# Kernel tuning notes

Hardware: AMD Instinct MI355X
Metric: run time of the kernel (lower is better)

The kernel has to match this reference:

```python
import jax, jax.numpy as jnp
import numpy as np
from jax import lax

B, T, V, E, H, L = 512, 128, 128, 512, 512, 2  # batch, seq, vocab, embd, hidden, layers


def setup_inputs() -> dict:
    key = jax.random.key(0)
    ks = jax.random.split(key, 6)
    s = 1.0 / np.sqrt(H)
    return {
        "input": jax.random.randint(ks[0], (B, T), 0, V),
        "encoder_curr_state": jnp.zeros((L, B, H), dtype=jnp.float32),
        "emb": jax.random.normal(ks[1], (V, E), dtype=jnp.float32) * 0.02,
        "w_ih": jax.random.uniform(ks[2], (L, 3 * H, E), minval=-s, maxval=s, dtype=jnp.float32),
        "w_hh": jax.random.uniform(ks[3], (L, 3 * H, H), minval=-s, maxval=s, dtype=jnp.float32),
        "b_ih": jax.random.uniform(ks[4], (L, 3 * H), minval=-s, maxval=s, dtype=jnp.float32),
        "b_hh": jax.random.uniform(ks[5], (L, 3 * H), minval=-s, maxval=s, dtype=jnp.float32),
    }


def _gru_cell(x, h, wi, wh, bi, bh):
    # torch GRU gate math: gates ordered (r, z, n)
    gi = x @ wi.T + bi  # [B, 3H]
    gh = h @ wh.T + bh  # [B, 3H]
    i_r, i_z, i_n = jnp.split(gi, 3, axis=-1)
    h_r, h_z, h_n = jnp.split(gh, 3, axis=-1)
    r = jax.nn.sigmoid(i_r + h_r)
    z = jax.nn.sigmoid(i_z + h_z)
    n = jnp.tanh(i_n + r * h_n)
    return (1.0 - z) * n + z * h


def reference(input, encoder_curr_state, emb, w_ih, w_hh, b_ih, b_hh):
    x_seq = emb[input]                      # [B, T, E]
    x_tbe = jnp.swapaxes(x_seq, 0, 1)       # [T, B, E]

    def step(h, x_t):
        hs = []
        inp = x_t
        for l in range(L):  # small fixed layer loop
            hl = _gru_cell(inp, h[l], w_ih[l], w_hh[l], b_ih[l], b_hh[l])
            hs.append(hl)
            inp = hl
        h_new = jnp.stack(hs)               # [L, B, H]
        return h_new, h_new

    h_final, states = lax.scan(step, encoder_curr_state, x_tbe)
    # states: [T, L, B, H] == encoder_states; h_final == encoder_curr_state after loop
    return states, h_final
```

## Files before the change

kernel.cpp:

```cpp
#include <hip/hip_runtime.h>
#include <hip/hip_bf16.h>
#include <math.h>


#define BB 512
#define TT 128
#define VV 128
#define EE 512
#define HH 512
#define LL 2
#define BH (BB*HH)

#define NBLK 192
#define GS   48

typedef short s16x8 __attribute__((ext_vector_type(8)));
typedef float f32x4 __attribute__((ext_vector_type(4)));

#define W_SZ    (3*HH*EE)
#define WH0_OFF 0
#define WI1_OFF (W_SZ)
#define WH1_OFF (2*W_SZ)
#define HBF_OFF (3*W_SZ)
#define HBF_SZ  (4*BH)
#define TBL_BYTE ((size_t)(3*W_SZ + HBF_SZ)*2)
#define TBL_SZ   (VV*3*HH)
#define BAR_BYTE (TBL_BYTE + (size_t)TBL_SZ*4)

#define MFMA(a,b,c) __builtin_amdgcn_mfma_f32_16x16x32_bf16((a),(b),(c),0,0,0)

#define PREP_N (3*W_SZ + 2*BH)
__global__ __launch_bounds__(256) void prep_bf16(
    const float* __restrict__ w_ih, const float* __restrict__ w_hh,
    const float* __restrict__ h0, __hip_bfloat16* __restrict__ wsb)
{
    const int i = blockIdx.x * 256 + threadIdx.x;
    if (i >= PREP_N) return;
    float v; int dst;
    if (i < W_SZ)            { v = w_hh[i];                 dst = i; }
    else if (i < 2*W_SZ)     { v = w_ih[W_SZ + i - W_SZ];   dst = i; }
    else if (i < 3*W_SZ)     { v = w_hh[W_SZ + i - 2*W_SZ]; dst = i; }
    else if (i < 3*W_SZ+BH)  { v = h0[i - 3*W_SZ];          dst = HBF_OFF + BH + (i - 3*W_SZ); }
    else                     { v = h0[i - 3*W_SZ];          dst = HBF_OFF + 3*BH + (i - 3*W_SZ - BH); }
    wsb[dst] = __float2bfloat16(v);
}

__global__ __launch_bounds__(256) void build_gi0(
    const float* __restrict__ emb, const float* __restrict__ w_ih,
    const float* __restrict__ b_ih, float* __restrict__ tbl)
{
    __shared__ __align__(16) float e[EE];
    const int v   = blockIdx.y;
    const int col = blockIdx.x * 256 + threadIdx.x;
    for (int i = threadIdx.x; i < EE; i += 256) e[i] = emb[v * EE + i];
    __syncthreads();
    const float4* w4 = (const float4*)(w_ih + (size_t)col * EE);
    const float4* e4 = (const float4*)e;
    float acc = 0.f;
    #pragma unroll 8
    for (int k = 0; k < EE/4; ++k) {
        float4 wv = w4[k], ev = e4[k];
        acc += wv.x*ev.x + wv.y*ev.y + wv.z*ev.z + wv.w*ev.w;
    }
    tbl[v * (3*HH) + col] = acc + b_ih[col];
}

__device__ __forceinline__ float sigm(float x) { return 1.f / (1.f + __expf(-x)); }
__device__ __forceinline__ float tanh_f(float x) {
    float e2 = __expf(2.f * x);
    return 1.f - 2.f / (e2 + 1.f);
}

__device__ __forceinline__ void grid_sync(unsigned* base) {
    asm volatile("s_waitcnt vmcnt(0)" ::: "memory");
    __syncthreads();
    if (threadIdx.x == 0) {
        unsigned* cnt = base;
        unsigned* gen = base + 32;
        unsigned* abt = base + 64;
        if (__hip_atomic_load(abt, __ATOMIC_RELAXED, __HIP_MEMORY_SCOPE_AGENT) == 0u) {
            unsigned g = __hip_atomic_load(gen, __ATOMIC_RELAXED, __HIP_MEMORY_SCOPE_AGENT);
            unsigned a = __hip_atomic_fetch_add(cnt, 1u, __ATOMIC_RELEASE, __HIP_MEMORY_SCOPE_AGENT);
            if (a == (unsigned)(GS - 1)) {
                __hip_atomic_store(cnt, 0u, __ATOMIC_RELAXED, __HIP_MEMORY_SCOPE_AGENT);
                __hip_atomic_store(gen, g + 1u, __ATOMIC_RELEASE, __HIP_MEMORY_SCOPE_AGENT);
            } else {
                int spins = 0;
                while (__hip_atomic_load(gen, __ATOMIC_RELAXED, __HIP_MEMORY_SCOPE_AGENT) == g) {
                    if (__hip_atomic_load(abt, __ATOMIC_RELAXED, __HIP_MEMORY_SCOPE_AGENT) != 0u)
                        break;
                    __builtin_amdgcn_s_sleep(2);
                    if (++spins > (1 << 20)) {
                        __hip_atomic_store(abt, 1u, __ATOMIC_RELAXED, __HIP_MEMORY_SCOPE_AGENT);
                        break;
                    }
                }
            }
        }
        __threadfence();
    }
    __syncthreads();
}

__global__ __launch_bounds__(512) void gru_persist(
    const int*   __restrict__ input,
    const float* __restrict__ h0,
    const float* __restrict__ b_ih,
    const float* __restrict__ b_hh,
    const __hip_bfloat16* __restrict__ wh0,
    const __hip_bfloat16* __restrict__ wi1,
    const __hip_bfloat16* __restrict__ wh1,
    const float* __restrict__ tbl,
    __hip_bfloat16* __restrict__ hbf,
    float*       __restrict__ out,
    unsigned*    __restrict__ bar)
{
    extern __shared__ __align__(16) char lds[];

    const int tid  = threadIdx.x;
    const int w    = tid >> 6;
    const int lane = tid & 63;
    const int l15  = lane & 15;
    const int lg   = lane >> 4;
    const int bid  = blockIdx.x;

    if (bid < 64) {
        const int bt = bid >> 4, ht = bid & 15;
        unsigned* gbar = bar + bt * 128;
        const int B0 = bt * 128 + w * 16;
        const int hbase = ht * 32;

        for (int j = 0; j < 12; ++j) {
            int cidx = tid + 512 * j;
            int lr = cidx >> 6, blk = cidx & 63;
            int g = lr >> 5, hl = lr & 31;
            s16x8 wv = *(const s16x8*)(wh0 + (size_t)(g*512 + hbase + hl)*512 + blk*8);
            *(s16x8*)(&lds[lr*1024 + ((blk ^ (lr & 7)) << 4)]) = wv;
        }
        __syncthreads();

        float bi_[2][3], bh_[2][3];
        #pragma unroll
        for (int nt = 0; nt < 2; ++nt) {
            const int h = hbase + nt*16 + l15;
            #pragma unroll
            for (int g = 0; g < 3; ++g) bh_[nt][g] = b_hh[g*512 + h];
        }
        (void)bi_;

        float hreg[2][4];
        #pragma unroll
        for (int nt = 0; nt < 2; ++nt)
            #pragma unroll
            for (int r = 0; r < 4; ++r)
                hreg[nt][r] = h0[(size_t)(B0 + lg*4 + r)*HH + hbase + nt*16 + l15];

        for (int t = 0; t < TT; ++t) {
            const __hip_bfloat16* hsrc = hbf + (size_t)((t + 1) & 1) * BH;

            float tv[2][3][4];
            #pragma unroll
            for (int r = 0; r < 4; ++r) {
                int vv = input[(B0 + lg*4 + r)*TT + t];
                const float* tp = tbl + (size_t)vv*(3*HH) + hbase + l15;
                #pragma unroll
                for (int g = 0; g < 3; ++g)
                    #pragma unroll
                    for (int nt = 0; nt < 2; ++nt)
                        tv[nt][g][r] = tp[g*512 + nt*16];
            }

            f32x4 acc[2][3];
            #pragma unroll
            for (int nt = 0; nt < 2; ++nt)
                #pragma unroll
                for (int g = 0; g < 3; ++g) acc[nt][g] = (f32x4)(0.f);

            #pragma unroll
            for (int c = 0; c < 16; ++c) {
                const s16x8 a = *(const s16x8*)(hsrc + (size_t)(B0 + l15)*512 + c*32 + lg*8);
                #pragma unroll
                for (int nt = 0; nt < 2; ++nt)
                    #pragma unroll
                    for (int g = 0; g < 3; ++g) {
                        int lr = g*32 + nt*16 + l15;
                        s16x8 bf = *(const s16x8*)(&lds[lr*1024 + (((c*4 + lg) ^ (lr & 7)) << 4)]);
                        acc[nt][g] = MFMA(a, bf, acc[nt][g]);
                    }
            }

            float* outp = out + (size_t)(t * 2) * BH;
            __hip_bfloat16* hw = hbf + (size_t)(t & 1) * BH;
            #pragma unroll
            for (int nt = 0; nt < 2; ++nt) {
                const int h = hbase + nt*16 + l15;
                #pragma unroll
                for (int r = 0; r < 4; ++r) {
                    const int b = B0 + lg*4 + r;
                    float rg = sigm(acc[nt][0][r] + tv[nt][0][r] + bh_[nt][0]);
                    float zg = sigm(acc[nt][1][r] + tv[nt][1][r] + bh_[nt][1]);
                    float ng = tanh_f(tv[nt][2][r] + rg*(acc[nt][2][r] + bh_[nt][2]));
                    float hn = (1.f - zg)*ng + zg*hreg[nt][r];
                    hreg[nt][r] = hn;
                    outp[(size_t)b*HH + h] = hn;
                    hw[(size_t)b*HH + h] = __float2bfloat16(hn);
                }
            }
            grid_sync(gbar);
        }
    } else {
        const int id = bid - 64;
        const int bt = id >> 5, ht = id & 31;
        unsigned* gbar = bar + bt * 128;
        const int B0 = bt * 128 + w * 16;
        const int hbase = ht * 16;

        for (int j = 0; j < 12; ++j) {
            int cidx = tid + 512 * j;
            int lr = cidx >> 7, blk = cidx & 127;
            int g = lr >> 4, hl = lr & 15;
            const __hip_bfloat16* src = (blk < 64) ? wi1 : wh1;
            s16x8 wv = *(const s16x8*)(src + (size_t)(g*512 + hbase + hl)*512 + (blk & 63)*8);
            *(s16x8*)(&lds[lr*2048 + ((blk ^ (lr & 7)) << 4)]) = wv;
        }
        __syncthreads();

        const int h = hbase + l15;
        const float bir = b_ih[1536 + h],       biz = b_ih[1536 + 512 + h],
                    bin = b_ih[1536 + 1024 + h];
        const float bhr = b_hh[1536 + h],       bhz = b_hh[1536 + 512 + h],
                    bhn = b_hh[1536 + 1024 + h];

        float hreg[4];
        #pragma unroll
        for (int r = 0; r < 4; ++r)
            hreg[r] = h0[(size_t)BH + (size_t)(B0 + lg*4 + r)*HH + h];

        grid_sync(gbar);
        for (int t = 0; t < TT; ++t) {
            const __hip_bfloat16* xsrc = hbf + (size_t)(t & 1) * BH;
            const __hip_bfloat16* hsrc = hbf + (size_t)(2 + ((t + 1) & 1)) * BH;
            f32x4 ar = (f32x4)(0.f), az = (f32x4)(0.f), ani = (f32x4)(0.f), anh = (f32x4)(0.f);

            #pragma unroll
            for (int c = 0; c < 32; ++c) {
                const __hip_bfloat16* asrc = (c < 16) ? xsrc : hsrc;
                const s16x8 a = *(const s16x8*)(asrc + (size_t)(B0 + l15)*512 + (c & 15)*32 + lg*8);
                int lr0 = 0*16 + l15, lr1 = 1*16 + l15, lr2 = 2*16 + l15;
                s16x8 b0 = *(const s16x8*)(&lds[lr0*2048 + (((c*4 + lg) ^ (lr0 & 7)) << 4)]);
                s16x8 b1 = *(const s16x8*)(&lds[lr1*2048 + (((c*4 + lg) ^ (lr1 & 7)) << 4)]);
                s16x8 b2 = *(const s16x8*)(&lds[lr2*2048 + (((c*4 + lg) ^ (lr2 & 7)) << 4)]);
                ar = MFMA(a, b0, ar);
                az = MFMA(a, b1, az);
                if (c < 16) ani = MFMA(a, b2, ani);
                else        anh = MFMA(a, b2, anh);
            }

            float* outp = out + (size_t)(t * 2 + 1) * BH;
            __hip_bfloat16* hw = hbf + (size_t)(2 + (t & 1)) * BH;
            #pragma unroll
            for (int r = 0; r < 4; ++r) {
                float rg = sigm(ar[r] + bir + bhr);
                float zg = sigm(az[r] + biz + bhz);
                float ng = tanh_f(ani[r] + bin + rg*(anh[r] + bhn));
                float hn = (1.f - zg)*ng + zg*hreg[r];
                hreg[r] = hn;
                int b = B0 + lg*4 + r;
                outp[(size_t)b*HH + h] = hn;
                hw[(size_t)b*HH + h] = __float2bfloat16(hn);
            }
            if (t < TT - 1) grid_sync(gbar);
        }
    }
}

__global__ __launch_bounds__(256) void copy_final(
    const float* __restrict__ states, float* __restrict__ dst)
{
    const int i = blockIdx.x * 256 + threadIdx.x;
    dst[i] = states[(size_t)(TT - 1) * LL * BH + i];
}

extern "C" void kernel_launch(void* const* d_in, const int* in_sizes, int n_in,
                              void* d_out, int out_size, void* d_ws, size_t ws_size,
                              hipStream_t stream) {
    const int*   input = (const int*)  d_in[0];
    const float* h0    = (const float*)d_in[1];
    const float* emb   = (const float*)d_in[2];
    const float* w_ih  = (const float*)d_in[3];
    const float* w_hh  = (const float*)d_in[4];
    const float* b_ih  = (const float*)d_in[5];
    const float* b_hh  = (const float*)d_in[6];
    float* out = (float*)d_out;

    __hip_bfloat16* wsb = (__hip_bfloat16*)d_ws;
    __hip_bfloat16* wh0 = wsb + WH0_OFF;
    __hip_bfloat16* wi1 = wsb + WI1_OFF;
    __hip_bfloat16* wh1 = wsb + WH1_OFF;
    __hip_bfloat16* hbf = wsb + HBF_OFF;
    float*    tbl = (float*)   ((char*)d_ws + TBL_BYTE);
    unsigned* bar = (unsigned*)((char*)d_ws + BAR_BYTE);

    hipMemsetAsync(bar, 0, 2048, stream);
    prep_bf16<<<(PREP_N + 255)/256, 256, 0, stream>>>(w_ih, w_hh, h0, wsb);
    build_gi0<<<dim3(6, VV), 256, 0, stream>>>(emb, w_ih, b_ih, tbl);

    gru_persist<<<NBLK, 512, 98304, stream>>>(input, h0, b_ih, b_hh,
                                              wh0, wi1, wh1, tbl, hbf, out, bar);

    copy_final<<<(LL*BH)/256, 256, 0, stream>>>(out, out + (size_t)TT * LL * BH);
}
```

Measured before the change: 2.682 ms.

## Streamline grid barrier with monotonic counter and coherent relaxed atomics for hidden state

Replaces the generation/reset grid barrier with a monotonic counter compared against an expected epoch, folds the abort flag into the generation word, and drops the sleep and threadfence. Hidden-state exchange now uses relaxed agent-scope atomic loads (prefetching all A fragments up front) and packed 32-bit atomic stores, so coherence comes from the atomics rather than from fences. It also adds a launch_bounds occupancy hint. The goal is lower per-step barrier latency across the 128 timesteps, at the cost of weaker memory-ordering guarantees that could allow stale reads.

```diff
diff --git a/kernel.cpp b/kernel.cpp
--- a/kernel.cpp
+++ b/kernel.cpp
@@ -13,6 +13,7 @@
 
 #define NBLK 192
 #define GS   48
+#define ABORT_BIT 0x80000000u
 
 typedef short s16x8 __attribute__((ext_vector_type(8)));
 typedef float f32x4 __attribute__((ext_vector_type(4)));
@@ -71,38 +72,49 @@
     return 1.f - 2.f / (e2 + 1.f);
 }
 
-__device__ __forceinline__ void grid_sync(unsigned* base) {
+__device__ __forceinline__ s16x8 gldc16(const __hip_bfloat16* p) {
+    union { struct { unsigned long long a, b; } q; s16x8 v; } u;
+    u.q.a = __hip_atomic_load((const unsigned long long*)p,
+                              __ATOMIC_RELAXED, __HIP_MEMORY_SCOPE_AGENT);
+    u.q.b = __hip_atomic_load(((const unsigned long long*)p) + 1,
+                              __ATOMIC_RELAXED, __HIP_MEMORY_SCOPE_AGENT);
+    return u.v;
+}
+
+__device__ __forceinline__ unsigned short bf16b(float f) {
+    union { __hip_bfloat16 h; unsigned short u; } u;
+    u.h = __float2bfloat16(f);
+    return u.u;
+}
+
+__device__ __forceinline__ void grid_sync(unsigned* base, unsigned k) {
     asm volatile("s_waitcnt vmcnt(0)" ::: "memory");
     __syncthreads();
     if (threadIdx.x == 0) {
         unsigned* cnt = base;
         unsigned* gen = base + 32;
-        unsigned* abt = base + 64;
-        if (__hip_atomic_load(abt, __ATOMIC_RELAXED, __HIP_MEMORY_SCOPE_AGENT) == 0u) {
-            unsigned g = __hip_atomic_load(gen, __ATOMIC_RELAXED, __HIP_MEMORY_SCOPE_AGENT);
-            unsigned a = __hip_atomic_fetch_add(cnt, 1u, __ATOMIC_RELEASE, __HIP_MEMORY_SCOPE_AGENT);
-            if (a == (unsigned)(GS - 1)) {
-                __hip_atomic_store(cnt, 0u, __ATOMIC_RELAXED, __HIP_MEMORY_SCOPE_AGENT);
-                __hip_atomic_store(gen, g + 1u, __ATOMIC_RELEASE, __HIP_MEMORY_SCOPE_AGENT);
+        unsigned v0 = __hip_atomic_load(gen, __ATOMIC_RELAXED, __HIP_MEMORY_SCOPE_AGENT);
+        if (!(v0 & ABORT_BIT)) {
+            unsigned a = __hip_atomic_fetch_add(cnt, 1u, __ATOMIC_RELAXED, __HIP_MEMORY_SCOPE_AGENT);
+            if (a == (unsigned)GS * k - 1u) {
+                __hip_atomic_store(gen, k, __ATOMIC_RELAXED, __HIP_MEMORY_SCOPE_AGENT);
             } else {
                 int spins = 0;
-                while (__hip_atomic_load(gen, __ATOMIC_RELAXED, __HIP_MEMORY_SCOPE_AGENT) == g) {
-                    if (__hip_atomic_load(abt, __ATOMIC_RELAXED, __HIP_MEMORY_SCOPE_AGENT) != 0u)
-                        break;
-                    __builtin_amdgcn_s_sleep(2);
-                    if (++spins > (1 << 20)) {
-                        __hip_atomic_store(abt, 1u, __ATOMIC_RELAXED, __HIP_MEMORY_SCOPE_AGENT);
+                for (;;) {
+                    unsigned v = __hip_atomic_load(gen, __ATOMIC_RELAXED, __HIP_MEMORY_SCOPE_AGENT);
+                    if ((v & ABORT_BIT) || v >= k) break;
+                    if (++spins > (1 << 21)) {
+                        __hip_atomic_store(gen, ABORT_BIT | k, __ATOMIC_RELAXED, __HIP_MEMORY_SCOPE_AGENT);
                         break;
                     }
                 }
             }
         }
-        __threadfence();
     }
     __syncthreads();
 }
 
-__global__ __launch_bounds__(512) void gru_persist(
+__global__ __launch_bounds__(512, 2) void gru_persist(
     const int*   __restrict__ input,
     const float* __restrict__ h0,
     const float* __restrict__ b_ih,
@@ -139,14 +151,12 @@
         }
         __syncthreads();
 
-        float bi_[2][3], bh_[2][3];
+        float bh_[2][3];
         #pragma unroll
-        for (int nt = 0; nt < 2; ++nt) {
-            const int h = hbase + nt*16 + l15;
-            #pragma unroll
-            for (int g = 0; g < 3; ++g) bh_[nt][g] = b_hh[g*512 + h];
-        }
-        (void)bi_;
+        for (int nt = 0; nt < 2; ++nt)
+            #pragma unroll
+            for (int g = 0; g < 3; ++g)
+                bh_[nt][g] = b_hh[g*512 + hbase + nt*16 + l15];
 
         float hreg[2][4];
         #pragma unroll
@@ -155,8 +165,14 @@
             for (int r = 0; r < 4; ++r)
                 hreg[nt][r] = h0[(size_t)(B0 + lg*4 + r)*HH + hbase + nt*16 + l15];
 
+        unsigned myk = 0;
         for (int t = 0; t < TT; ++t) {
             const __hip_bfloat16* hsrc = hbf + (size_t)((t + 1) & 1) * BH;
+
+            s16x8 a[16];
+            #pragma unroll
+            for (int c = 0; c < 16; ++c)
+                a[c] = gldc16(hsrc + (size_t)(B0 + l15)*512 + c*32 + lg*8);
 
             float tv[2][3][4];
             #pragma unroll
@@ -177,23 +193,21 @@
                 for (int g = 0; g < 3; ++g) acc[nt][g] = (f32x4)(0.f);
 
             #pragma unroll
-            for (int c = 0; c < 16; ++c) {
-                const s16x8 a = *(const s16x8*)(hsrc + (size_t)(B0 + l15)*512 + c*32 + lg*8);
+            for (int c = 0; c < 16; ++c)
                 #pragma unroll
                 for (int nt = 0; nt < 2; ++nt)
                     #pragma unroll
                     for (int g = 0; g < 3; ++g) {
                         int lr = g*32 + nt*16 + l15;
                         s16x8 bf = *(const s16x8*)(&lds[lr*1024 + (((c*4 + lg) ^ (lr & 7)) << 4)]);
-                        acc[nt][g] = MFMA(a, bf, acc[nt][g]);
+                        acc[nt][g] = MFMA(a[c], bf, acc[nt][g]);
                     }
-            }
 
             float* outp = out + (size_t)(t * 2) * BH;
             __hip_bfloat16* hw = hbf + (size_t)(t & 1) * BH;
             #pragma unroll
             for (int nt = 0; nt < 2; ++nt) {
-                const int h = hbase + nt*16 + l15;
+                const int hcol = hbase + nt*16 + l15;
                 #pragma unroll
                 for (int r = 0; r < 4; ++r) {
                     const int b = B0 + lg*4 + r;
@@ -202,11 +216,16 @@
                     float ng = tanh_f(tv[nt][2][r] + rg*(acc[nt][2][r] + bh_[nt][2]));
                     float hn = (1.f - zg)*ng + zg*hreg[nt][r];
                     hreg[nt][r] = hn;
-                    outp[(size_t)b*HH + h] = hn;
-                    hw[(size_t)b*HH + h] = __float2bfloat16(hn);
+                    outp[(size_t)b*HH + hcol] = hn;
+                    float nb = __shfl_down(hn, 1);
+                    if ((l15 & 1) == 0) {
+                        unsigned pv = (unsigned)bf16b(hn) | ((unsigned)bf16b(nb) << 16);
+                        __hip_atomic_store((unsigned*)(hw + (size_t)b*HH + hcol), pv,
+                                           __ATOMIC_RELAXED, __HIP_MEMORY_SCOPE_AGENT);
+                    }
                 }
             }
-            grid_sync(gbar);
+            grid_sync(gbar, ++myk);
         }
     } else {
         const int id = bid - 64;
@@ -225,35 +244,41 @@
         }
         __syncthreads();
 
-        const int h = hbase + l15;
-        const float bir = b_ih[1536 + h],       biz = b_ih[1536 + 512 + h],
-                    bin = b_ih[1536 + 1024 + h];
-        const float bhr = b_hh[1536 + h],       bhz = b_hh[1536 + 512 + h],
-                    bhn = b_hh[1536 + 1024 + h];
+        const int hcol = hbase + l15;
+        const float bir = b_ih[1536 + hcol],       biz = b_ih[1536 + 512 + hcol],
+                    bin = b_ih[1536 + 1024 + hcol];
+        const float bhr = b_hh[1536 + hcol],       bhz = b_hh[1536 + 512 + hcol],
+                    bhn = b_hh[1536 + 1024 + hcol];
 
         float hreg[4];
         #pragma unroll
         for (int r = 0; r < 4; ++r)
-            hreg[r] = h0[(size_t)BH + (size_t)(B0 + lg*4 + r)*HH + h];
-
-        grid_sync(gbar);
+            hreg[r] = h0[(size_t)BH + (size_t)(B0 + lg*4 + r)*HH + hcol];
+
+        unsigned myk = 0;
+        grid_sync(gbar, ++myk);
         for (int t = 0; t < TT; ++t) {
             const __hip_bfloat16* xsrc = hbf + (size_t)(t & 1) * BH;
             const __hip_bfloat16* hsrc = hbf + (size_t)(2 + ((t + 1) & 1)) * BH;
-            f32x4 ar = (f32x4)(0.f), az = (f32x4)(0.f), ani = (f32x4)(0.f), anh = (f32x4)(0.f);
-
+
+            s16x8 aa[32];
             #pragma unroll
             for (int c = 0; c < 32; ++c) {
                 const __hip_bfloat16* asrc = (c < 16) ? xsrc : hsrc;
-                const s16x8 a = *(const s16x8*)(asrc + (size_t)(B0 + l15)*512 + (c & 15)*32 + lg*8);
-                int lr0 = 0*16 + l15, lr1 = 1*16 + l15, lr2 = 2*16 + l15;
+                aa[c] = gldc16(asrc + (size_t)(B0 + l15)*512 + (c & 15)*32 + lg*8);
+            }
+
+            f32x4 ar = (f32x4)(0.f), az = (f32x4)(0.f), ani = (f32x4)(0.f), anh = (f32x4)(0.f);
+            #pragma unroll
+            for (int c = 0; c < 32; ++c) {
+                int lr0 = l15, lr1 = 16 + l15, lr2 = 32 + l15;
                 s16x8 b0 = *(const s16x8*)(&lds[lr0*2048 + (((c*4 + lg) ^ (lr0 & 7)) << 4)]);
                 s16x8 b1 = *(const s16x8*)(&lds[lr1*2048 + (((c*4 + lg) ^ (lr1 & 7)) << 4)]);
                 s16x8 b2 = *(const s16x8*)(&lds[lr2*2048 + (((c*4 + lg) ^ (lr2 & 7)) << 4)]);
-                ar = MFMA(a, b0, ar);
-                az = MFMA(a, b1, az);
-                if (c < 16) ani = MFMA(a, b2, ani);
-                else        anh = MFMA(a, b2, anh);
+                ar = MFMA(aa[c], b0, ar);
+                az = MFMA(aa[c], b1, az);
+                if (c < 16) ani = MFMA(aa[c], b2, ani);
+                else        anh = MFMA(aa[c], b2, anh);
             }
 
             float* outp = out + (size_t)(t * 2 + 1) * BH;
@@ -266,10 +291,15 @@
                 float hn = (1.f - zg)*ng + zg*hreg[r];
                 hreg[r] = hn;
                 int b = B0 + lg*4 + r;
-                outp[(size_t)b*HH + h] = hn;
-                hw[(size_t)b*HH + h] = __float2bfloat16(hn);
-            }
-            if (t < TT - 1) grid_sync(gbar);
+                outp[(size_t)b*HH + hcol] = hn;
+                float nb = __shfl_down(hn, 1);
+                if ((l15 & 1) == 0) {
+                    unsigned pv = (unsigned)bf16b(hn) | ((unsigned)bf16b(nb) << 16);
+                    __hip_atomic_store((unsigned*)(hw + (size_t)b*HH + hcol), pv,
+                                       __ATOMIC_RELAXED, __HIP_MEMORY_SCOPE_AGENT);
+                }
+            }
+            if (t < TT - 1) grid_sync(gbar, ++myk);
         }
     }
 }
```

Result: faster. 2.522 ms (-6.0%).
